# Kernel tuning notes

Hardware: AMD Instinct MI355X
Metric: run time of the kernel (lower is better)

Reference implementation:

```python
import jax, jax.numpy as jnp
import numpy as np

N, C = 1048576, 128
ALPHA, GAMA = 0.25, 2


def setup_inputs() -> dict:
    key = jax.random.key(0)
    k1, k2 = jax.random.split(key)
    preds = jax.random.normal(k1, (N, C), dtype=jnp.float32)
    label_idx = jax.random.randint(k2, (N,), 0, C)
    labels = jax.nn.one_hot(label_idx, C, dtype=jnp.int32)  # one-hot, matches labels[i][j]==1 test
    return {"preds": preds, "labels": labels}


def reference(preds, labels):
    # t2[i] = -preds[i, label_i]  (gather via one-hot)
    lbl_logit = jnp.sum(preds * labels.astype(preds.dtype), axis=1)  # [N]
    t2 = -lbl_logit
    # t1[i] = sum_j exp(preds[i, j])  (original uses unstabilized sum-exp)
    t1 = jnp.sum(jnp.exp(preds), axis=1)  # [N]
    # per-row focal loss: alpha * (1 - p)^gama * CE, with p = exp(label_logit)/sumexp
    p = jnp.exp(-t2) / t1
    per_row = ALPHA * jnp.power(1.0 - p, GAMA) * (t2 + jnp.log(t1))
    # the final python loop is an incremental running mean => plain mean
    return jnp.mean(per_row)
```

## Files before the change

kernel.cpp:

```cpp
#include <hip/hip_runtime.h>

#define FL_N 1048576
#define FL_C 128
#define FL_ALPHA 0.25f

constexpr int BLOCKS = 1024;
constexpr int TPB    = 256;
constexpr int WAVES_PER_BLOCK = TPB / 64;

__global__ __launch_bounds__(TPB) void focal_partial(
    const float* __restrict__ preds,
    const int*   __restrict__ labels,
    float*       __restrict__ partial)
{
    const int tid  = threadIdx.x;
    const int wave = tid >> 6;
    const int lane = tid & 63;
    const int sub  = lane & 31;

    const int wavesTotal = gridDim.x * WAVES_PER_BLOCK;
    const int gwave      = blockIdx.x * WAVES_PER_BLOCK + wave;

    float acc = 0.0f;

    for (int rp = gwave; rp < FL_N / 2; rp += wavesTotal) {
        size_t base = (size_t)rp * (2 * FL_C) + (size_t)lane * 4;
        float4 p = *reinterpret_cast<const float4*>(preds + base);
        int4   l = *reinterpret_cast<const int4*>(labels + base);

        float se = __expf(p.x) + __expf(p.y) + __expf(p.z) + __expf(p.w);
        float ll = p.x * (float)l.x + p.y * (float)l.y
                 + p.z * (float)l.z + p.w * (float)l.w;

        #pragma unroll
        for (int m = 16; m >= 1; m >>= 1) {
            se += __shfl_xor(se, m, 64);
            ll += __shfl_xor(ll, m, 64);
        }

        if (sub == 0) {
            float t1 = se;
            float pp = __expf(ll) / t1;
            float om = 1.0f - pp;
            acc += FL_ALPHA * om * om * (__logf(t1) - ll);
        }
    }

    #pragma unroll
    for (int m = 32; m >= 1; m >>= 1)
        acc += __shfl_xor(acc, m, 64);

    __shared__ float smem[WAVES_PER_BLOCK];
    if (lane == 0) smem[wave] = acc;
    __syncthreads();
    if (tid == 0) {
        float s = 0.0f;
        #pragma unroll
        for (int w = 0; w < WAVES_PER_BLOCK; ++w) s += smem[w];
        partial[blockIdx.x] = s;
    }
}

__global__ __launch_bounds__(256) void focal_final(
    const float* __restrict__ partial,
    float*       __restrict__ out)
{
    const int tid  = threadIdx.x;
    const int wave = tid >> 6;
    const int lane = tid & 63;

    float acc = 0.0f;
    for (int i = tid; i < BLOCKS; i += 256) acc += partial[i];

    #pragma unroll
    for (int m = 32; m >= 1; m >>= 1)
        acc += __shfl_xor(acc, m, 64);

    __shared__ float smem[4];
    if (lane == 0) smem[wave] = acc;
    __syncthreads();
    if (tid == 0) {
        float s = smem[0] + smem[1] + smem[2] + smem[3];
        out[0] = s * (1.0f / (float)FL_N);
    }
}

extern "C" void kernel_launch(void* const* d_in, const int* in_sizes, int n_in,
                              void* d_out, int out_size, void* d_ws, size_t ws_size,
                              hipStream_t stream)
{
    const float* preds  = (const float*)d_in[0];
    const int*   labels = (const int*)d_in[1];
    float*       out    = (float*)d_out;
    float*       part   = (float*)d_ws;

    focal_partial<<<BLOCKS, TPB, 0, stream>>>(preds, labels, part);
    focal_final<<<1, 256, 0, stream>>>(part, out);
}
```

Baseline: 964.2 us.

## Process eight rows per wave with four nontemporal vector loads per lane

Each wave now handles eight rows per iteration, with 8 lanes per row and each lane loading four float4/int4 chunks. Loads use nontemporal hints, which cuts the cross-lane shuffle reduction from 5 steps to 3 and keeps more bytes in flight per lane. The block count doubles to 2048. The per-lane access pattern is strided by 32 bytes within a row, so coalescing per instruction is lower, and register use rises.

```diff
diff --git a/kernel.cpp b/kernel.cpp
--- a/kernel.cpp
+++ b/kernel.cpp
@@ -4,9 +4,21 @@
 #define FL_C 128
 #define FL_ALPHA 0.25f
 
-constexpr int BLOCKS = 1024;
+constexpr int BLOCKS = 2048;
 constexpr int TPB    = 256;
 constexpr int WAVES_PER_BLOCK = TPB / 64;
+constexpr int ROWS_PER_WAVE   = 8;
+constexpr int ROWBLOCKS       = FL_N / ROWS_PER_WAVE;
+
+using f32x4 = __attribute__((ext_vector_type(4))) float;
+using i32x4 = __attribute__((ext_vector_type(4))) int;
+
+__device__ __forceinline__ float exp4_sum(f32x4 p) {
+    return __expf(p.x) + __expf(p.y) + __expf(p.z) + __expf(p.w);
+}
+__device__ __forceinline__ float dot4(f32x4 p, i32x4 l) {
+    return p.x * (float)l.x + p.y * (float)l.y + p.z * (float)l.z + p.w * (float)l.w;
+}
 
 __global__ __launch_bounds__(TPB) void focal_partial(
     const float* __restrict__ preds,
@@ -16,32 +28,41 @@
     const int tid  = threadIdx.x;
     const int wave = tid >> 6;
     const int lane = tid & 63;
-    const int sub  = lane & 31;
 
     const int wavesTotal = gridDim.x * WAVES_PER_BLOCK;
     const int gwave      = blockIdx.x * WAVES_PER_BLOCK + wave;
 
+    const int laneOff = (lane >> 3) * FL_C + (lane & 7) * 4;
+
     float acc = 0.0f;
 
-    for (int rp = gwave; rp < FL_N / 2; rp += wavesTotal) {
-        size_t base = (size_t)rp * (2 * FL_C) + (size_t)lane * 4;
-        float4 p = *reinterpret_cast<const float4*>(preds + base);
-        int4   l = *reinterpret_cast<const int4*>(labels + base);
+    for (int rb = gwave; rb < ROWBLOCKS; rb += wavesTotal) {
+        size_t base = (size_t)rb * (ROWS_PER_WAVE * FL_C) + laneOff;
+        const f32x4* pp = reinterpret_cast<const f32x4*>(preds + base);
+        const i32x4* lp = reinterpret_cast<const i32x4*>(labels + base);
 
-        float se = __expf(p.x) + __expf(p.y) + __expf(p.z) + __expf(p.w);
-        float ll = p.x * (float)l.x + p.y * (float)l.y
-                 + p.z * (float)l.z + p.w * (float)l.w;
+        f32x4 p0 = __builtin_nontemporal_load(pp + 0);
+        f32x4 p1 = __builtin_nontemporal_load(pp + 8);
+        f32x4 p2 = __builtin_nontemporal_load(pp + 16);
+        f32x4 p3 = __builtin_nontemporal_load(pp + 24);
+        i32x4 l0 = __builtin_nontemporal_load(lp + 0);
+        i32x4 l1 = __builtin_nontemporal_load(lp + 8);
+        i32x4 l2 = __builtin_nontemporal_load(lp + 16);
+        i32x4 l3 = __builtin_nontemporal_load(lp + 24);
+
+        float se = exp4_sum(p0) + exp4_sum(p1) + exp4_sum(p2) + exp4_sum(p3);
+        float ll = dot4(p0, l0) + dot4(p1, l1) + dot4(p2, l2) + dot4(p3, l3);
 
         #pragma unroll
-        for (int m = 16; m >= 1; m >>= 1) {
+        for (int m = 4; m >= 1; m >>= 1) {
             se += __shfl_xor(se, m, 64);
             ll += __shfl_xor(ll, m, 64);
         }
 
-        if (sub == 0) {
+        if ((lane & 7) == 0) {
             float t1 = se;
-            float pp = __expf(ll) / t1;
-            float om = 1.0f - pp;
+            float pr = __expf(ll) / t1;
+            float om = 1.0f - pr;
             acc += FL_ALPHA * om * om * (__logf(t1) - ll);
         }
     }
```

After: 927.7 us. 1.04x faster.
